# Kernel tuning notes

Hardware: AMD Instinct MI355X
Metric: run time of the kernel (lower is better)

## Reference

```python
import jax, jax.numpy as jnp
import numpy as np

SEQ = 16384
HID = 1280
HEADS = 16
HEAD_DIM = HID // HEADS  # 80
NUM_WIN = 16
WIN = SEQ // NUM_WIN  # 1024


def rotate_half(x):
    x1, x2 = jnp.split(x, 2, axis=-1)
    return jnp.concatenate([-x2, x1], axis=-1)


def setup_inputs() -> dict:
    key = jax.random.key(0)
    ks = jax.random.split(key, 8)
    pos = jnp.arange(SEQ, dtype=jnp.float32)[:, None]
    inv_freq = 1.0 / (10000.0 ** (jnp.arange(0, HEAD_DIM, 2, dtype=jnp.float32) / HEAD_DIM))
    ang = pos * inv_freq[None, :]
    ang = jnp.concatenate([ang, ang], axis=-1)  # [SEQ, HEAD_DIM]
    return {
        "hidden_states": jax.random.normal(ks[0], (SEQ, HID), dtype=jnp.float32),
        "cos": jnp.cos(ang),
        "sin": jnp.sin(ang),
        "qkv_kernel": jax.random.normal(ks[1], (HID, 3 * HID), dtype=jnp.float32) * 0.02,
        "qkv_bias": jnp.zeros((3 * HID,), dtype=jnp.float32),
        "proj_kernel": jax.random.normal(ks[2], (HID, HID), dtype=jnp.float32) * 0.02,
        "proj_bias": jnp.zeros((HID,), dtype=jnp.float32),
        "cu_seqlens": jnp.arange(NUM_WIN + 1, dtype=jnp.int32) * WIN,
    }


def reference(hidden_states, cos, sin, qkv_kernel, qkv_bias, proj_kernel, proj_bias, cu_seqlens):
    seq_len = hidden_states.shape[0]
    scale = HEAD_DIM ** (-0.5)
    qkv = hidden_states @ qkv_kernel + qkv_bias
    q, k, v = jnp.split(qkv, 3, axis=-1)
    q = q.reshape(seq_len, HEADS, HEAD_DIM)
    k = k.reshape(seq_len, HEADS, HEAD_DIM)
    v = v.reshape(seq_len, HEADS, HEAD_DIM)
    c = cos[:, None, :HEAD_DIM]
    s = sin[:, None, :HEAD_DIM]
    q = q * c + rotate_half(q) * s
    k = k * c + rotate_half(k) * s
    num_win = cu_seqlens.shape[0] - 1
    win = seq_len // num_win
    qw = q.reshape(num_win, win, HEADS, HEAD_DIM).astype(jnp.float32)
    kw = k.reshape(num_win, win, HEADS, HEAD_DIM).astype(jnp.float32)
    vw = v.reshape(num_win, win, HEADS, HEAD_DIM).astype(jnp.float32)
    scores = jnp.einsum('wqhd,wkhd->whqk', qw, kw) * scale
    weights = jax.nn.softmax(scores, axis=-1)
    out = jnp.einsum('whqk,wkhd->wqhd', weights, vw)
    out = out.reshape(seq_len, HID)
    return out @ proj_kernel + proj_bias
```

## Files before the change

### kernel.cpp

```cpp
#include <hip/hip_runtime.h>
#include <stdint.h>

#define SEQ 16384
#define HIDN 1280
#define NHEADS 16
#define HD 80
#define HDP 96
#define NWIN 16
#define WINSZ 1024

typedef unsigned short u16;
typedef unsigned int u32;
typedef __bf16 bf16x8 __attribute__((ext_vector_type(8)));
typedef float f32x4 __attribute__((ext_vector_type(4)));

#define AS1 __attribute__((address_space(1)))
#define AS3 __attribute__((address_space(3)))

__device__ __forceinline__ u16 f2b(float f) {
  __bf16 h = (__bf16)f;
  return __builtin_bit_cast(u16, h);
}
__device__ __forceinline__ u32 f2b2(float lo, float hi) {
  __bf16 l = (__bf16)lo, h = (__bf16)hi;
  return (u32)__builtin_bit_cast(u16, l) | ((u32)__builtin_bit_cast(u16, h) << 16);
}
__device__ __forceinline__ float b2f(u16 u) { return __uint_as_float(((u32)u) << 16); }

__device__ __forceinline__ float fexp2(float x) {
#if __has_builtin(__builtin_amdgcn_exp2f)
  return __builtin_amdgcn_exp2f(x);
#else
  return exp2f(x);
#endif
}

__device__ __forceinline__ void load_lds16(const void* g, void* l) {
  __builtin_amdgcn_global_load_lds((AS1 void*)g, (AS3 void*)l, 16, 0, 0);
}

__global__ void k_cvt(const float* __restrict__ in, u16* __restrict__ out) {
  size_t i = ((size_t)blockIdx.x * 256 + threadIdx.x) * 4;
  float4 v = *(const float4*)(in + i);
  uint2 o;
  o.x = f2b2(v.x, v.y);
  o.y = f2b2(v.z, v.w);
  *(uint2*)(out + i) = o;
}

__global__ void k_trans(const float* __restrict__ in, u16* __restrict__ out, int R, int C) {
  __shared__ float tile[64][65];
  int c0 = blockIdx.x * 64, r0 = blockIdx.y * 64;
  int tc = threadIdx.x & 63, tr4 = threadIdx.x >> 6;
#pragma unroll
  for (int i = 0; i < 16; i++) {
    int r = tr4 + i * 4;
    tile[r][tc] = in[(size_t)(r0 + r) * C + c0 + tc];
  }
  __syncthreads();
#pragma unroll
  for (int i = 0; i < 16; i++) {
    int r = tr4 + i * 4;
    out[(size_t)(c0 + r) * R + r0 + tc] = f2b(tile[tc][r]);
  }
}

template <int MODE>
__launch_bounds__(1024, 4)
__global__ void k_gemm(const u16* __restrict__ A, const u16* __restrict__ B,
                       const float* __restrict__ bias, float* __restrict__ outf,
                       u16* __restrict__ Qb, u16* __restrict__ Kb, u16* __restrict__ Vt,
                       int N, int K, int ncol) {
  __shared__ char lds[65536];
  const int tid = threadIdx.x;
  const int wv = tid >> 6, lane = tid & 63;
  const int lr = lane & 15, lq = lane >> 4;
  const int wm = wv >> 2, wn = wv & 3;
  const int id = blockIdx.x;
  const int xs = id & 7, rest = id >> 3;
  const int cb = rest % ncol, rs = rest / ncol;
  const int row0 = (rs * 8 + xs) * 256, col0 = cb * 256;

  const u16* gsrc[2];
  int loff[2];
#pragma unroll
  for (int i = 0; i < 2; i++) {
    int g = 2 * wv + i;
    if (g < 16) {
      gsrc[i] = A + (size_t)(row0 + g * 16 + lr) * K + lq * 8;
      loff[i] = g * 1024 + lane * 16;
    } else {
      gsrc[i] = B + (size_t)(col0 + (g - 16) * 16 + lr) * K + lq * 8;
      loff[i] = 16384 + (g - 16) * 1024 + lane * 16;
    }
  }

  f32x4 acc[4][4];
#pragma unroll
  for (int i = 0; i < 4; i++)
#pragma unroll
    for (int j = 0; j < 4; j++) acc[i][j] = (f32x4){0.f, 0.f, 0.f, 0.f};

  const int nk = K >> 5;
#pragma unroll
  for (int i = 0; i < 2; i++) load_lds16(gsrc[i], lds + loff[i]);

  int buf = 0;
  for (int it = 0; it < nk; it++) {
    __syncthreads();
    if (it + 1 < nk) {
      int koff = (it + 1) * 32;
#pragma unroll
      for (int i = 0; i < 2; i++)
        load_lds16(gsrc[i] + koff, lds + (buf ^ 1) * 32768 + loff[i]);
    }
    const char* la = lds + buf * 32768;
    bf16x8 af[4], bfr[4];
#pragma unroll
    for (int mi = 0; mi < 4; mi++)
      af[mi] = *(const bf16x8*)(la + (wm * 4 + mi) * 1024 + lane * 16);
#pragma unroll
    for (int ni = 0; ni < 4; ni++)
      bfr[ni] = *(const bf16x8*)(la + 16384 + (wn * 4 + ni) * 1024 + lane * 16);
#pragma unroll
    for (int mi = 0; mi < 4; mi++)
#pragma unroll
      for (int ni = 0; ni < 4; ni++)
        acc[mi][ni] = __builtin_amdgcn_mfma_f32_16x16x32_bf16(af[mi], bfr[ni], acc[mi][ni], 0, 0, 0);
    buf ^= 1;
  }

#pragma unroll
  for (int ni = 0; ni < 4; ni++) {
    int col = col0 + wn * 64 + ni * 16 + lr;
    float bs = bias[col];
    if (MODE == 0) {
#pragma unroll
      for (int mi = 0; mi < 4; mi++)
#pragma unroll
        for (int r = 0; r < 4; r++) {
          int row = row0 + wm * 64 + mi * 16 + lq * 4 + r;
          outf[(size_t)row * N + col] = acc[mi][ni][r] + bs;
        }
    } else {
      int seg = col / HIDN;
      int cl = col - seg * HIDN;
      int h = cl / HD, d = cl - h * HD;
      if (seg == 2) {
#pragma unroll
        for (int mi = 0; mi < 4; mi++) {
          int row = row0 + wm * 64 + mi * 16 + lq * 4;
          uint2 o;
          o.x = f2b2(acc[mi][ni][0] + bs, acc[mi][ni][1] + bs);
          o.y = f2b2(acc[mi][ni][2] + bs, acc[mi][ni][3] + bs);
          *(uint2*)(Vt + ((size_t)h * HD + d) * SEQ + row) = o;
        }
      } else {
        u16* Dst = (seg == 0) ? Qb : Kb;
#pragma unroll
        for (int mi = 0; mi < 4; mi++)
#pragma unroll
          for (int r = 0; r < 4; r++) {
            int row = row0 + wm * 64 + mi * 16 + lq * 4 + r;
            Dst[((size_t)h * SEQ + row) * HDP + d] = f2b(acc[mi][ni][r] + bs);
          }
      }
    }
  }
}

__global__ void k_rope2(u16* __restrict__ Q, u16* __restrict__ K,
                        const float* __restrict__ cs, const float* __restrict__ sn) {
  int idx = blockIdx.x * 256 + threadIdx.x;
  const int TOT = NHEADS * SEQ * 10;
  u16* X = Q;
  if (idx >= TOT) { X = K; idx -= TOT; }
  int h = idx / (SEQ * 10);
  int rem = idx - h * (SEQ * 10);
  int s = rem / 10;
  int t = rem - s * 10;
  int d = t * 4;
  size_t base = ((size_t)h * SEQ + s) * HDP;
  float4 cv = *(const float4*)(cs + s * HD + d);
  float4 sv = *(const float4*)(sn + s * HD + d);
  uint2 a = *(const uint2*)(X + base + d);
  uint2 b = *(const uint2*)(X + base + d + 40);
  float x1[4], x2[4];
  x1[0] = b2f(a.x & 0xffffu); x1[1] = b2f(a.x >> 16);
  x1[2] = b2f(a.y & 0xffffu); x1[3] = b2f(a.y >> 16);
  x2[0] = b2f(b.x & 0xffffu); x2[1] = b2f(b.x >> 16);
  x2[2] = b2f(b.y & 0xffffu); x2[3] = b2f(b.y >> 16);
  uint2 o1, o2;
  o1.x = f2b2(x1[0] * cv.x - x2[0] * sv.x, x1[1] * cv.y - x2[1] * sv.y);
  o1.y = f2b2(x1[2] * cv.z - x2[2] * sv.z, x1[3] * cv.w - x2[3] * sv.w);
  o2.x = f2b2(x2[0] * cv.x + x1[0] * sv.x, x2[1] * cv.y + x1[1] * sv.y);
  o2.y = f2b2(x2[2] * cv.z + x1[2] * sv.z, x2[3] * cv.w + x1[3] * sv.w);
  *(uint2*)(X + base + d) = o1;
  *(uint2*)(X + base + d + 40) = o2;
  if (t < 4) {
    uint2 z; z.x = 0; z.y = 0;
    *(uint2*)(X + base + 80 + t * 4) = z;
  }
}

__launch_bounds__(256, 2)
__global__ void k_attn(const u16* __restrict__ Qb, const u16* __restrict__ Kb,
                       const u16* __restrict__ Vt, u16* __restrict__ Ob) {
  __shared__ char lds[24576 + 20480 + 4 * 4352];
  char* ldsK = lds;
  char* ldsV = lds + 24576;
  char* ldsP = lds + 45056;

  const int tid = threadIdx.x;
  const int wv = tid >> 6, lane = tid & 63;
  const int lr = lane & 15, lq = lane >> 4;

  const int b = blockIdx.x;
  const int qblk = b & 7, h = (b >> 3) & 15, w = b >> 7;
  const int q0 = w * WINSZ + qblk * 128 + wv * 32;
  const int kwin = w * WINSZ;

  bf16x8 qf[2][3];
#pragma unroll
  for (int qt = 0; qt < 2; qt++)
#pragma unroll
    for (int ds = 0; ds < 3; ds++)
      qf[qt][ds] = *(const bf16x8*)(Qb + ((size_t)h * SEQ + q0 + qt * 16 + lr) * HDP + ds * 32 + lq * 8);

  f32x4 acc[2][5];
#pragma unroll
  for (int i = 0; i < 2; i++)
#pragma unroll
    for (int j = 0; j < 5; j++) acc[i][j] = (f32x4){0.f, 0.f, 0.f, 0.f};
  float mo[2] = {-1e30f, -1e30f};
  float lsum[2] = {0.f, 0.f};
  const float kscale = 0.11180339887498949f * 1.4426950408889634f;

  for (int kt = 0; kt < 8; kt++) {
    int k0 = kwin + kt * 128;
#pragma unroll
    for (int li = 0; li < 11; li++) {
      int g = li * 4 + wv;
      const u16* gp;
      char* lp;
      if (g < 24) {
        int kt16 = g / 3, ds = g - kt16 * 3;
        gp = Kb + ((size_t)h * SEQ + k0 + kt16 * 16 + lr) * HDP + ds * 32 + lq * 8;
        lp = ldsK + g * 1024;
      } else {
        int g2 = g - 24;
        int dt = g2 >> 2, ks = g2 & 3;
        gp = Vt + ((size_t)h * HD + dt * 16 + lr) * SEQ + k0 + ks * 32 + lq * 8;
        lp = ldsV + g2 * 1024;
      }
      load_lds16(gp, lp);
    }
    __syncthreads();

    f32x4 sx[2][8];
#pragma unroll
    for (int i = 0; i < 2; i++)
#pragma unroll
      for (int j = 0; j < 8; j++) sx[i][j] = (f32x4){0.f, 0.f, 0.f, 0.f};
    __builtin_amdgcn_s_setprio(1);
#pragma unroll
    for (int kt16 = 0; kt16 < 8; kt16++) {
      bf16x8 kf0 = *(const bf16x8*)(ldsK + (kt16 * 3 + 0) * 1024 + lane * 16);
      bf16x8 kf1 = *(const bf16x8*)(ldsK + (kt16 * 3 + 1) * 1024 + lane * 16);
      bf16x8 kf2 = *(const bf16x8*)(ldsK + (kt16 * 3 + 2) * 1024 + lane * 16);
#pragma unroll
      for (int qt = 0; qt < 2; qt++) {
        sx[qt][kt16] = __builtin_amdgcn_mfma_f32_16x16x32_bf16(kf0, qf[qt][0], sx[qt][kt16], 0, 0, 0);
        sx[qt][kt16] = __builtin_amdgcn_mfma_f32_16x16x32_bf16(kf1, qf[qt][1], sx[qt][kt16], 0, 0, 0);
        sx[qt][kt16] = __builtin_amdgcn_mfma_f32_16x16x32_bf16(kf2, qf[qt][2], sx[qt][kt16], 0, 0, 0);
      }
    }
    __builtin_amdgcn_s_setprio(0);

    bf16x8 pf[2][4];
#pragma unroll
    for (int qt = 0; qt < 2; qt++) {
      float mx = -1e30f;
#pragma unroll
      for (int t = 0; t < 8; t++)
#pragma unroll
        for (int r = 0; r < 4; r++) mx = fmaxf(mx, sx[qt][t][r]);
      mx = fmaxf(mx, __shfl_xor(mx, 16));
      mx = fmaxf(mx, __shfl_xor(mx, 32));
      float mxs = mx * kscale;
      if (!__all(mxs <= mo[qt] + 8.f)) {
        float mnew = fmaxf(mo[qt], mxs);
        float alpha = fexp2(mo[qt] - mnew);
        mo[qt] = mnew;
        lsum[qt] *= alpha;
#pragma unroll
        for (int dt = 0; dt < 5; dt++) acc[qt][dt] *= alpha;
      }
      float ls = 0.f;
#pragma unroll
      for (int t = 0; t < 8; t++)
#pragma unroll
        for (int r = 0; r < 4; r++) {
          float p = fexp2(fmaf(sx[qt][t][r], kscale, -mo[qt]));
          sx[qt][t][r] = p;
          ls += p;
        }
      ls += __shfl_xor(ls, 16);
      ls += __shfl_xor(ls, 32);
      lsum[qt] += ls;
      char* pw = ldsP + wv * 4352;
#pragma unroll
      for (int t = 0; t < 8; t++) {
        uint2 o;
        o.x = f2b2(sx[qt][t][0], sx[qt][t][1]);
        o.y = f2b2(sx[qt][t][2], sx[qt][t][3]);
        *(uint2*)(pw + lr * 272 + t * 32 + lq * 8) = o;
      }
#pragma unroll
      for (int ks = 0; ks < 4; ks++)
        pf[qt][ks] = *(const bf16x8*)(pw + lr * 272 + ks * 64 + lq * 16);
    }

    __builtin_amdgcn_s_setprio(1);
#pragma unroll
    for (int dt = 0; dt < 5; dt++)
#pragma unroll
      for (int ks = 0; ks < 4; ks++) {
        bf16x8 vf = *(const bf16x8*)(ldsV + (dt * 4 + ks) * 1024 + lane * 16);
#pragma unroll
        for (int qt = 0; qt < 2; qt++)
          acc[qt][dt] = __builtin_amdgcn_mfma_f32_16x16x32_bf16(vf, pf[qt][ks], acc[qt][dt], 0, 0, 0);
      }
    __builtin_amdgcn_s_setprio(0);
    __syncthreads();
  }

#pragma unroll
  for (int qt = 0; qt < 2; qt++) {
    float rl = 1.f / lsum[qt];
    int s = q0 + qt * 16 + lr;
#pragma unroll
    for (int dt = 0; dt < 5; dt++) {
      uint2 o;
      o.x = f2b2(acc[qt][dt][0] * rl, acc[qt][dt][1] * rl);
      o.y = f2b2(acc[qt][dt][2] * rl, acc[qt][dt][3] * rl);
      size_t ob = (size_t)s * HIDN + h * HD + dt * 16 + lq * 4;
      *(uint2*)(Ob + ob) = o;
    }
  }
}

extern "C" void kernel_launch(void* const* d_in, const int* in_sizes, int n_in,
                              void* d_out, int out_size, void* d_ws, size_t ws_size,
                              hipStream_t stream) {
  (void)in_sizes; (void)n_in; (void)out_size; (void)ws_size;
  const float* hidden = (const float*)d_in[0];
  const float* cosb   = (const float*)d_in[1];
  const float* sinb   = (const float*)d_in[2];
  const float* qkvk   = (const float*)d_in[3];
  const float* qkvb   = (const float*)d_in[4];
  const float* projk  = (const float*)d_in[5];
  const float* projb  = (const float*)d_in[6];

  char* ws = (char*)d_ws;
  u16* Abf = (u16*)(ws + 0);
  u16* Wt  = (u16*)(ws + 41943040);
  u16* Pt  = (u16*)(ws + 51773440);
  u16* Qb  = (u16*)(ws + 55050240);
  u16* Kb  = (u16*)(ws + 105381888);
  u16* Vtb = (u16*)(ws + 155713536);

  k_cvt<<<20480, 256, 0, stream>>>(hidden, Abf);
  k_trans<<<dim3(60, 20), 256, 0, stream>>>(qkvk, Wt, 1280, 3840);
  k_trans<<<dim3(20, 20), 256, 0, stream>>>(projk, Pt, 1280, 1280);
  k_gemm<1><<<960, 1024, 0, stream>>>(Abf, Wt, qkvb, nullptr, Qb, Kb, Vtb, 3840, 1280, 15);
  k_rope2<<<20480, 256, 0, stream>>>(Qb, Kb, cosb, sinb);
  k_attn<<<2048, 256, 0, stream>>>(Qb, Kb, Vtb, Abf);
  k_gemm<0><<<320, 1024, 0, stream>>>(Abf, Pt, projb, (float*)d_out,
                                      nullptr, nullptr, nullptr, 1280, 1280, 5);
}
```

Before: 686.9 us.

## Rewrite GEMM as 8-wave kernel with swizzled LDS and deeper K pipeline

Replaces the 1024-thread GEMM with a 512-thread (8-wave) kernel in which each wave computes 128x64 (8x4 MFMA tiles). It uses 128KB of dynamic LDS with XOR-swizzled layout, K-tiles of 64 split into halves, and a multi-stage prefetch with explicit vmcnt waits, raw s_barrier, and s_setprio around the MFMA bursts. The goal is better overlap of global loads with matrix math and fewer LDS bank conflicts. In exchange it uses more registers for the larger accumulator set, allows less occupancy, and hardcodes K=1280.

```diff
diff --git a/kernel.cpp b/kernel.cpp
--- a/kernel.cpp
+++ b/kernel.cpp
@@ -65,13 +65,18 @@
   }
 }
 
+
+#define GBAR() asm volatile("s_barrier" ::: "memory")
+
 template <int MODE>
-__launch_bounds__(1024, 4)
-__global__ void k_gemm(const u16* __restrict__ A, const u16* __restrict__ B,
-                       const float* __restrict__ bias, float* __restrict__ outf,
-                       u16* __restrict__ Qb, u16* __restrict__ Kb, u16* __restrict__ Vt,
-                       int N, int K, int ncol) {
-  __shared__ char lds[65536];
+__launch_bounds__(512, 2)
+__global__ void k_gemm8(const u16* __restrict__ A, const u16* __restrict__ B,
+                        const float* __restrict__ bias, float* __restrict__ outf,
+                        u16* __restrict__ Qb, u16* __restrict__ Kb, u16* __restrict__ Vt,
+                        int N, int ncol) {
+  extern __shared__ char lds[];
+  const int K = 1280;
+  const int NT = 20;
   const int tid = threadIdx.x;
   const int wv = tid >> 6, lane = tid & 63;
   const int lr = lane & 15, lq = lane >> 4;
@@ -81,54 +86,130 @@
   const int cb = rest % ncol, rs = rest / ncol;
   const int row0 = (rs * 8 + xs) * 256, col0 = cb * 256;
 
-  const u16* gsrc[2];
-  int loff[2];
-#pragma unroll
-  for (int i = 0; i < 2; i++) {
-    int g = 2 * wv + i;
-    if (g < 16) {
-      gsrc[i] = A + (size_t)(row0 + g * 16 + lr) * K + lq * 8;
-      loff[i] = g * 1024 + lane * 16;
-    } else {
-      gsrc[i] = B + (size_t)(col0 + (g - 16) * 16 + lr) * K + lq * 8;
-      loff[i] = 16384 + (g - 16) * 1024 + lane * 16;
-    }
-  }
-
-  f32x4 acc[4][4];
-#pragma unroll
-  for (int i = 0; i < 4; i++)
+  const u16* gA[2];
+  const u16* gB[2];
+  int Pst[2];
+#pragma unroll
+  for (int ld = 0; ld < 2; ld++) {
+    int P = wv * 2048 + ld * 1024 + lane * 16;
+    int j = P >> 7;
+    int Wl = (P & 127) ^ ((j & 7) << 4);
+    int r = 2 * j + (Wl >> 6);
+    int c = (Wl & 63) >> 1;
+    gA[ld] = A + (size_t)(row0 + r) * K + c;
+    gB[ld] = B + (size_t)(col0 + r) * K + c;
+    Pst[ld] = P;
+  }
+
+  int offA[2][4], offB[4];
+#pragma unroll
+  for (int ch = 0; ch < 2; ch++)
+#pragma unroll
+    for (int a = 0; a < 4; a++) {
+      int r = wm * 128 + ch * 64 + a * 16 + lr;
+      int j = r >> 1;
+      int Wl = ((r & 1) << 6) | (lq << 4);
+      offA[ch][a] = j * 128 + (Wl ^ ((j & 7) << 4));
+    }
+#pragma unroll
+  for (int ni = 0; ni < 4; ni++) {
+    int r = wn * 64 + ni * 16 + lr;
+    int j = r >> 1;
+    int Wl = ((r & 1) << 6) | (lq << 4);
+    offB[ni] = 32768 + j * 128 + (Wl ^ ((j & 7) << 4));
+  }
+
+  f32x4 acc[8][4];
+#pragma unroll
+  for (int i = 0; i < 8; i++)
 #pragma unroll
     for (int j = 0; j < 4; j++) acc[i][j] = (f32x4){0.f, 0.f, 0.f, 0.f};
 
-  const int nk = K >> 5;
-#pragma unroll
-  for (int i = 0; i < 2; i++) load_lds16(gsrc[i], lds + loff[i]);
-
-  int buf = 0;
-  for (int it = 0; it < nk; it++) {
-    __syncthreads();
-    if (it + 1 < nk) {
-      int koff = (it + 1) * 32;
-#pragma unroll
-      for (int i = 0; i < 2; i++)
-        load_lds16(gsrc[i] + koff, lds + (buf ^ 1) * 32768 + loff[i]);
-    }
-    const char* la = lds + buf * 32768;
-    bf16x8 af[4], bfr[4];
-#pragma unroll
-    for (int mi = 0; mi < 4; mi++)
-      af[mi] = *(const bf16x8*)(la + (wm * 4 + mi) * 1024 + lane * 16);
-#pragma unroll
-    for (int ni = 0; ni < 4; ni++)
-      bfr[ni] = *(const bf16x8*)(la + 16384 + (wn * 4 + ni) * 1024 + lane * 16);
-#pragma unroll
-    for (int mi = 0; mi < 4; mi++)
+#define STAGE(mat_, kh_, kt_)                                        \
+  do {                                                               \
+    char* lb_ = lds + (((kt_) & 1) << 16) + ((mat_) << 15) + ((kh_) << 14); \
+    const u16* g0_ = (mat_) ? gB[0] : gA[0];                         \
+    const u16* g1_ = (mat_) ? gB[1] : gA[1];                         \
+    int ko_ = (kt_) * 64 + (kh_) * 32;                               \
+    load_lds16(g0_ + ko_, lb_ + Pst[0]);                             \
+    load_lds16(g1_ + ko_, lb_ + Pst[1]);                             \
+  } while (0)
+
+  STAGE(0, 0, 0);
+  STAGE(1, 0, 0);
+  STAGE(0, 1, 0);
+  STAGE(1, 1, 0);
+  STAGE(0, 0, 1);
+  STAGE(1, 0, 1);
+  asm volatile("s_waitcnt vmcnt(4)" ::: "memory");
+  GBAR();
+
+#pragma unroll 2
+  for (int t = 0; t < NT; t++) {
+    const int bb = (t & 1) << 16;
+    bf16x8 bfr[4], afr[4];
+
+#pragma unroll
+    for (int ni = 0; ni < 4; ni++) bfr[ni] = *(const bf16x8*)(lds + bb + offB[ni]);
+#pragma unroll
+    for (int a = 0; a < 4; a++) afr[a] = *(const bf16x8*)(lds + bb + offA[0][a]);
+    if (t + 1 < NT) STAGE(0, 1, t + 1);
+    GBAR();
+    __builtin_amdgcn_s_setprio(1);
+#pragma unroll
+    for (int a = 0; a < 4; a++)
 #pragma unroll
       for (int ni = 0; ni < 4; ni++)
-        acc[mi][ni] = __builtin_amdgcn_mfma_f32_16x16x32_bf16(af[mi], bfr[ni], acc[mi][ni], 0, 0, 0);
-    buf ^= 1;
-  }
+        acc[a][ni] = __builtin_amdgcn_mfma_f32_16x16x32_bf16(afr[a], bfr[ni], acc[a][ni], 0, 0, 0);
+    __builtin_amdgcn_s_setprio(0);
+    GBAR();
+
+#pragma unroll
+    for (int a = 0; a < 4; a++) afr[a] = *(const bf16x8*)(lds + bb + offA[1][a]);
+    if (t + 1 < NT) STAGE(1, 1, t + 1);
+    GBAR();
+    __builtin_amdgcn_s_setprio(1);
+#pragma unroll
+    for (int a = 0; a < 4; a++)
+#pragma unroll
+      for (int ni = 0; ni < 4; ni++)
+        acc[4 + a][ni] = __builtin_amdgcn_mfma_f32_16x16x32_bf16(afr[a], bfr[ni], acc[4 + a][ni], 0, 0, 0);
+    __builtin_amdgcn_s_setprio(0);
+    GBAR();
+
+#pragma unroll
+    for (int ni = 0; ni < 4; ni++) bfr[ni] = *(const bf16x8*)(lds + bb + 16384 + offB[ni]);
+#pragma unroll
+    for (int a = 0; a < 4; a++) afr[a] = *(const bf16x8*)(lds + bb + 16384 + offA[0][a]);
+    if (t + 2 < NT) STAGE(0, 0, t + 2);
+    GBAR();
+    __builtin_amdgcn_s_setprio(1);
+#pragma unroll
+    for (int a = 0; a < 4; a++)
+#pragma unroll
+      for (int ni = 0; ni < 4; ni++)
+        acc[a][ni] = __builtin_amdgcn_mfma_f32_16x16x32_bf16(afr[a], bfr[ni], acc[a][ni], 0, 0, 0);
+    __builtin_amdgcn_s_setprio(0);
+    GBAR();
+
+#pragma unroll
+    for (int a = 0; a < 4; a++) afr[a] = *(const bf16x8*)(lds + bb + 16384 + offA[1][a]);
+    if (t + 2 < NT) STAGE(1, 0, t + 2);
+    if (t < NT - 2)
+      asm volatile("s_waitcnt vmcnt(4)" ::: "memory");
+    else if (t == NT - 2)
+      asm volatile("s_waitcnt vmcnt(0)" ::: "memory");
+    GBAR();
+    __builtin_amdgcn_s_setprio(1);
+#pragma unroll
+    for (int a = 0; a < 4; a++)
+#pragma unroll
+      for (int ni = 0; ni < 4; ni++)
+        acc[4 + a][ni] = __builtin_amdgcn_mfma_f32_16x16x32_bf16(afr[a], bfr[ni], acc[4 + a][ni], 0, 0, 0);
+    __builtin_amdgcn_s_setprio(0);
+    GBAR();
+  }
+#undef STAGE
 
 #pragma unroll
   for (int ni = 0; ni < 4; ni++) {
@@ -136,10 +217,10 @@
     float bs = bias[col];
     if (MODE == 0) {
 #pragma unroll
-      for (int mi = 0; mi < 4; mi++)
+      for (int mi = 0; mi < 8; mi++)
 #pragma unroll
         for (int r = 0; r < 4; r++) {
-          int row = row0 + wm * 64 + mi * 16 + lq * 4 + r;
+          int row = row0 + wm * 128 + mi * 16 + lq * 4 + r;
           outf[(size_t)row * N + col] = acc[mi][ni][r] + bs;
         }
     } else {
@@ -148,8 +229,8 @@
       int h = cl / HD, d = cl - h * HD;
       if (seg == 2) {
 #pragma unroll
-        for (int mi = 0; mi < 4; mi++) {
-          int row = row0 + wm * 64 + mi * 16 + lq * 4;
+        for (int mi = 0; mi < 8; mi++) {
+          int row = row0 + wm * 128 + mi * 16 + lq * 4;
           uint2 o;
           o.x = f2b2(acc[mi][ni][0] + bs, acc[mi][ni][1] + bs);
           o.y = f2b2(acc[mi][ni][2] + bs, acc[mi][ni][3] + bs);
@@ -158,10 +239,10 @@
       } else {
         u16* Dst = (seg == 0) ? Qb : Kb;
 #pragma unroll
-        for (int mi = 0; mi < 4; mi++)
+        for (int mi = 0; mi < 8; mi++)
 #pragma unroll
           for (int r = 0; r < 4; r++) {
-            int row = row0 + wm * 64 + mi * 16 + lq * 4 + r;
+            int row = row0 + wm * 128 + mi * 16 + lq * 4 + r;
             Dst[((size_t)h * SEQ + row) * HDP + d] = f2b(acc[mi][ni][r] + bs);
           }
       }
@@ -370,12 +451,22 @@
   u16* Kb  = (u16*)(ws + 105381888);
   u16* Vtb = (u16*)(ws + 155713536);
 
+  static int attr_done = 0;
+  if (!attr_done) {
+    (void)hipFuncSetAttribute((const void*)&k_gemm8<1>,
+                              hipFuncAttributeMaxDynamicSharedMemorySize, 131072);
+    (void)hipFuncSetAttribute((const void*)&k_gemm8<0>,
+                              hipFuncAttributeMaxDynamicSharedMemorySize, 131072);
+    (void)hipGetLastError();
+    attr_done = 1;
+  }
+
   k_cvt<<<20480, 256, 0, stream>>>(hidden, Abf);
   k_trans<<<dim3(60, 20), 256, 0, stream>>>(qkvk, Wt, 1280, 3840);
   k_trans<<<dim3(20, 20), 256, 0, stream>>>(projk, Pt, 1280, 1280);
-  k_gemm<1><<<960, 1024, 0, stream>>>(Abf, Wt, qkvb, nullptr, Qb, Kb, Vtb, 3840, 1280, 15);
+  k_gemm8<1><<<960, 512, 131072, stream>>>(Abf, Wt, qkvb, nullptr, Qb, Kb, Vtb, 3840, 15);
   k_rope2<<<20480, 256, 0, stream>>>(Qb, Kb, cosb, sinb);
   k_attn<<<2048, 256, 0, stream>>>(Qb, Kb, Vtb, Abf);
-  k_gemm<0><<<320, 1024, 0, stream>>>(Abf, Pt, projb, (float*)d_out,
-                                      nullptr, nullptr, nullptr, 1280, 1280, 5);
-}
+  k_gemm8<0><<<320, 512, 131072, stream>>>(Abf, Pt, projb, (float*)d_out,
+                                           nullptr, nullptr, nullptr, 1280, 5);
+}
```

Measured after the change: 639.7 us. -6.9%, faster.
